# Performance work log

Hardware: AMD Instinct MI355X
Metric: run time of the kernel (lower is better)

The kernel has to match this reference:

```python
import jax, jax.numpy as jnp
import numpy as np

T, B, I, H = 4096, 32, 128, 128


def setup_inputs() -> dict:
    key = jax.random.key(0)
    ks = jax.random.split(key, 8)
    return {
        "input": jax.random.normal(ks[0], (T, B, I), dtype=jnp.float32),
        "h0": jax.random.normal(ks[1], (B, H), dtype=jnp.float32),
        "c0": jax.random.normal(ks[2], (B, H), dtype=jnp.float32),
        "noise": jax.random.normal(ks[3], (B, H), dtype=jnp.float32),
        "W_ih": jax.random.normal(ks[4], (4 * H, I), dtype=jnp.float32) * 0.05,
        "W_hh": jax.random.normal(ks[5], (4 * H, H), dtype=jnp.float32) * 0.05,
        "b_ih": jax.random.normal(ks[6], (4 * H,), dtype=jnp.float32) * 0.05,
        "b_hh": jax.random.normal(ks[7], (4 * H,), dtype=jnp.float32) * 0.05,
    }


def reference(input, h0, c0, noise, W_ih, W_hh, b_ih, b_hh):
    # NOTE: the source LSTMLayer never rebinds `state` inside its loop, so every
    # timestep applies the cell to the SAME initial (h0, c0). This is therefore a
    # time-batched (non-recurrent) LSTM-cell application -> fully vectorized over T.
    hsz = h0.shape[-1]
    # gates: [T, B, 4H]
    gates = (
        jnp.einsum("tbi,gi->tbg", input, W_ih)
        + jnp.einsum("bh,gh->bg", h0, W_hh)[None, :, :]
        + (b_ih + b_hh)
    )
    i_g = jax.nn.sigmoid(gates[..., 0 * hsz : 1 * hsz])
    f_g = jax.nn.sigmoid(gates[..., 1 * hsz : 2 * hsz])
    g_g = jnp.tanh(gates[..., 2 * hsz : 3 * hsz])
    o_g = jax.nn.sigmoid(gates[..., 3 * hsz : 4 * hsz])
    c = f_g * c0[None] + i_g * g_g               # [T, B, H]
    h = o_g * jnp.tanh(c) + noise[None]          # [T, B, H] (additive process noise)
    outputs = h
    # (h, c) returned by the torch loop are those of the LAST iteration
    return (outputs, (h[-1], c[-1]))
```

## Files before the change

kernel.cpp:

```cpp
#include <hip/hip_runtime.h>
#include <hip/hip_bf16.h>

#define T_DIM 4096
#define B_DIM 32
#define H_DIM 128
#define M_DIM (T_DIM * B_DIM)
#define G_DIM 512
#define TBH   ((long)M_DIM * H_DIM)

#define RPB    512
#define NCHUNK (RPB / 32)
#define LSTR   136
#define LBUF   (32 * LSTR)

typedef __attribute__((ext_vector_type(8))) short short8;
typedef __attribute__((ext_vector_type(4))) short short4v;
typedef __attribute__((ext_vector_type(4))) float floatx4;

__device__ __forceinline__ unsigned short f2bf_rne(float x) {
    union { float f; unsigned int u; } v; v.f = x;
    unsigned int r = v.u + 0x7FFFu + ((v.u >> 16) & 1u);
    return (unsigned short)(r >> 16);
}
__device__ __forceinline__ unsigned short f2bf_rh(float x) {
    union { float f; unsigned int u; } v; v.f = x;
    return (unsigned short)((v.u + 0x8000u) >> 16);
}
__device__ __forceinline__ float ex2(float x) { return __builtin_amdgcn_exp2f(x); }
__device__ __forceinline__ float rcpf(float x) { return __builtin_amdgcn_rcpf(x); }
__device__ __forceinline__ short8 pack8(float4 f0, float4 f1) {
    short8 s;
    s[0] = (short)f2bf_rh(f0.x); s[1] = (short)f2bf_rh(f0.y);
    s[2] = (short)f2bf_rh(f0.z); s[3] = (short)f2bf_rh(f0.w);
    s[4] = (short)f2bf_rh(f1.x); s[5] = (short)f2bf_rh(f1.y);
    s[6] = (short)f2bf_rh(f1.z); s[7] = (short)f2bf_rh(f1.w);
    return s;
}

__global__ void prep(const float* __restrict__ h0,
                     const float* __restrict__ W_hh,
                     const float* __restrict__ b_ih,
                     const float* __restrict__ b_hh,
                     const float* __restrict__ W_ih,
                     unsigned short* __restrict__ Wb,
                     float* __restrict__ hh) {
    const int tid = threadIdx.x;
    if (blockIdx.x < 32) {
        __shared__ float h0s[128];
        const int b = blockIdx.x;
        if (tid < 128) h0s[tid] = h0[b * 128 + tid];
        __syncthreads();
        for (int g = tid; g < G_DIM; g += 256) {
            float acc = b_ih[g] + b_hh[g];
            const float* wr = W_hh + g * 128;
            #pragma unroll 8
            for (int k = 0; k < 128; ++k) acc += wr[k] * h0s[k];
            hh[b * G_DIM + g] = acc;
        }
    } else {
        const int e = ((blockIdx.x - 32) * 256 + tid) * 4;
        float4 f = *(const float4*)(W_ih + e);
        short4v s;
        s[0] = (short)f2bf_rne(f.x); s[1] = (short)f2bf_rne(f.y);
        s[2] = (short)f2bf_rne(f.z); s[3] = (short)f2bf_rne(f.w);
        *(short4v*)(Wb + e) = s;
    }
}

__global__ __launch_bounds__(512, 2) void lstm_main(
    const float* __restrict__ X,
    const unsigned short* __restrict__ W,
    const float* __restrict__ hh,
    const float* __restrict__ c0,
    const float* __restrict__ noise,
    float* __restrict__ out)
{
    __shared__ unsigned short Xs[2 * LBUF];

    const int tid  = threadIdx.x;
    const int w    = tid >> 6;
    const int lane = tid & 63;
    const int q    = lane >> 4;
    const int lr   = lane & 15;
    const int hcol = (w << 4) + lr;
    const long row0 = (long)blockIdx.x * RPB;

    short8 wf[4][4];
    #pragma unroll
    for (int g = 0; g < 4; ++g)
        #pragma unroll
        for (int kt = 0; kt < 4; ++kt)
            wf[g][kt] = *(const short8*)(W + (g * 128 + hcol) * 128 + kt * 32 + q * 8);

    floatx4 hhf[2][4];
    float c0v[2][4], nzv[2][4];
    #pragma unroll
    for (int mt = 0; mt < 2; ++mt) {
        #pragma unroll
        for (int r = 0; r < 4; ++r) {
            const int b = mt * 16 + q * 4 + r;
            c0v[mt][r] = c0[b * 128 + hcol];
            nzv[mt][r] = noise[b * 128 + hcol];
        }
        #pragma unroll
        for (int g = 0; g < 4; ++g) {
            floatx4 a;
            #pragma unroll
            for (int r = 0; r < 4; ++r)
                a[r] = hh[(mt * 16 + q * 4 + r) * G_DIM + g * 128 + hcol];
            hhf[mt][g] = a;
        }
    }

    const int srow = tid >> 4;
    const int scol = (tid & 15) << 3;
    const float* xsrc = X + (row0 + srow) * 128 + scol;
    unsigned short* lws = &Xs[srow * LSTR + scol];

    {
        float4 f0 = *(const float4*)(xsrc);
        float4 f1 = *(const float4*)(xsrc + 4);
        *(short8*)lws = pack8(f0, f1);
    }
    float4 p0 = *(const float4*)(xsrc + 4096);
    float4 p1 = *(const float4*)(xsrc + 4096 + 4);
    __syncthreads();

    const float K1  = 1.44269504f;
    const float K2  = 2.88539008f;

    for (int c = 0; c < NCHUNK; ++c) {
        float4 n0 = {}, n1 = {};
        if (c + 2 < NCHUNK) {
            n0 = *(const float4*)(xsrc + (long)(c + 2) * 4096);
            n1 = *(const float4*)(xsrc + (long)(c + 2) * 4096 + 4);
        }

        const unsigned short* rb = &Xs[(c & 1) * LBUF];
        short8 af[2][4];
        #pragma unroll
        for (int mt = 0; mt < 2; ++mt)
            #pragma unroll
            for (int kt = 0; kt < 4; ++kt)
                af[mt][kt] = *(const short8*)(rb + (mt * 16 + lr) * LSTR + kt * 32 + q * 8);

        floatx4 acc[2][4];
        #pragma unroll
        for (int g = 0; g < 4; ++g) {
            acc[0][g] = __builtin_amdgcn_mfma_f32_16x16x32_bf16(af[0][0], wf[g][0], hhf[0][g], 0, 0, 0);
            acc[1][g] = __builtin_amdgcn_mfma_f32_16x16x32_bf16(af[1][0], wf[g][0], hhf[1][g], 0, 0, 0);
        }
        #pragma unroll
        for (int kt = 1; kt < 4; ++kt)
            #pragma unroll
            for (int g = 0; g < 4; ++g) {
                acc[0][g] = __builtin_amdgcn_mfma_f32_16x16x32_bf16(af[0][kt], wf[g][kt], acc[0][g], 0, 0, 0);
                acc[1][g] = __builtin_amdgcn_mfma_f32_16x16x32_bf16(af[1][kt], wf[g][kt], acc[1][g], 0, 0, 0);
            }

        const long rbase = row0 + (long)c * 32;
        const bool last = (rbase == M_DIM - 32);
        #pragma unroll
        for (int mt = 0; mt < 2; ++mt)
            #pragma unroll
            for (int r = 0; r < 4; ++r) {
                const long row = rbase + mt * 16 + q * 4 + r;
                const float ai = acc[mt][0][r];
                const float af_ = acc[mt][1][r];
                const float ag = acc[mt][2][r];
                const float ao = acc[mt][3][r];
                const float Ei = ex2(-K1 * ai);
                const float Ef = ex2(-K1 * af_);
                const float Eg = ex2( K2 * ag);
                const float Eo = ex2(-K1 * ao);
                const float ig = (Eg - 1.0f) * rcpf((1.0f + Ei) * (Eg + 1.0f));
                const float gf = rcpf(1.0f + Ef);
                const float cc = __builtin_fmaf(gf, c0v[mt][r], ig);
                const float Ec = ex2( K2 * cc);
                const float ot = (Ec - 1.0f) * rcpf((1.0f + Eo) * (Ec + 1.0f));
                const float hv = ot + nzv[mt][r];
                out[row * 128 + hcol] = hv;
                if (last) {
                    const int b = mt * 16 + q * 4 + r;
                    out[TBH +        b * 128 + hcol] = hv;
                    out[TBH + 4096 + b * 128 + hcol] = cc;
                }
            }

        if (c + 1 < NCHUNK)
            *(short8*)(lws + ((c + 1) & 1) * LBUF) = pack8(p0, p1);
        __syncthreads();
        p0 = n0; p1 = n1;
    }
}

extern "C" void kernel_launch(void* const* d_in, const int* in_sizes, int n_in,
                              void* d_out, int out_size, void* d_ws, size_t ws_size,
                              hipStream_t stream) {
    const float* X     = (const float*)d_in[0];
    const float* h0    = (const float*)d_in[1];
    const float* c0    = (const float*)d_in[2];
    const float* noise = (const float*)d_in[3];
    const float* W_ih  = (const float*)d_in[4];
    const float* W_hh  = (const float*)d_in[5];
    const float* b_ih  = (const float*)d_in[6];
    const float* b_hh  = (const float*)d_in[7];

    unsigned short* Wb = (unsigned short*)d_ws;
    float* hh = (float*)((char*)d_ws + 512 * 128 * sizeof(unsigned short));
    float* out = (float*)d_out;

    prep<<<dim3(96), dim3(256), 0, stream>>>(h0, W_hh, b_ih, b_hh, W_ih, Wb, hh);
    lstm_main<<<dim3(M_DIM / RPB), dim3(512), 0, stream>>>(X, Wb, hh, c0, noise, out);
}
```

Before: 149.7 us.

## Split LSTM gate computation across specialized wave groups with LDS handoff

Blocks grow to 1024 threads. Waves 0-7 compute the input and cell-candidate gates, convert the next X chunk to bf16 and write i*g to a double-buffered shared array. Waves 8-15 compute the forget and output gates, read i*g after the barrier, and do the cell/hidden activation and the global stores. This halves per-wave MFMA, register and transcendental work, and separates the load and store roles. The cost is extra LDS traffic, one more shared buffer, and a tighter coupling between the two wave groups at each barrier.

```diff
diff --git a/kernel.cpp b/kernel.cpp
--- a/kernel.cpp
+++ b/kernel.cpp
@@ -12,6 +12,9 @@
 #define NCHUNK (RPB / 32)
 #define LSTR   136
 #define LBUF   (32 * LSTR)
+#define IGSTR  20
+#define IGPAIR (32 * IGSTR)
+#define IGBUF  (8 * IGPAIR)
 
 typedef __attribute__((ext_vector_type(8))) short short8;
 typedef __attribute__((ext_vector_type(4))) short short4v;
@@ -67,7 +70,7 @@
     }
 }
 
-__global__ __launch_bounds__(512, 2) void lstm_main(
+__global__ __launch_bounds__(1024) void lstm_main(
     const float* __restrict__ X,
     const unsigned short* __restrict__ W,
     const float* __restrict__ hh,
@@ -76,40 +79,47 @@
     float* __restrict__ out)
 {
     __shared__ unsigned short Xs[2 * LBUF];
+    __shared__ float igs[2 * IGBUF];
 
     const int tid  = threadIdx.x;
     const int w    = tid >> 6;
     const int lane = tid & 63;
     const int q    = lane >> 4;
     const int lr   = lane & 15;
-    const int hcol = (w << 4) + lr;
+    const bool isA = (w < 8);
+    const int p    = w & 7;
+    const int bsel = w >> 3;
+    const int hcol = (p << 4) + lr;
     const long row0 = (long)blockIdx.x * RPB;
 
-    short8 wf[4][4];
+    short8 wf[2][4];
     #pragma unroll
-    for (int g = 0; g < 4; ++g)
+    for (int j = 0; j < 2; ++j)
         #pragma unroll
         for (int kt = 0; kt < 4; ++kt)
-            wf[g][kt] = *(const short8*)(W + (g * 128 + hcol) * 128 + kt * 32 + q * 8);
-
-    floatx4 hhf[2][4];
+            wf[j][kt] = *(const short8*)(W + (((j << 1) | bsel) * 128 + hcol) * 128 + kt * 32 + q * 8);
+
+    floatx4 hhf[2][2];
+    #pragma unroll
+    for (int mt = 0; mt < 2; ++mt)
+        #pragma unroll
+        for (int j = 0; j < 2; ++j) {
+            floatx4 a;
+            #pragma unroll
+            for (int r = 0; r < 4; ++r)
+                a[r] = hh[(mt * 16 + q * 4 + r) * G_DIM + ((j << 1) | bsel) * 128 + hcol];
+            hhf[mt][j] = a;
+        }
     float c0v[2][4], nzv[2][4];
-    #pragma unroll
-    for (int mt = 0; mt < 2; ++mt) {
-        #pragma unroll
-        for (int r = 0; r < 4; ++r) {
-            const int b = mt * 16 + q * 4 + r;
-            c0v[mt][r] = c0[b * 128 + hcol];
-            nzv[mt][r] = noise[b * 128 + hcol];
-        }
-        #pragma unroll
-        for (int g = 0; g < 4; ++g) {
-            floatx4 a;
-            #pragma unroll
-            for (int r = 0; r < 4; ++r)
-                a[r] = hh[(mt * 16 + q * 4 + r) * G_DIM + g * 128 + hcol];
-            hhf[mt][g] = a;
-        }
+    if (!isA) {
+        #pragma unroll
+        for (int mt = 0; mt < 2; ++mt)
+            #pragma unroll
+            for (int r = 0; r < 4; ++r) {
+                const int b = mt * 16 + q * 4 + r;
+                c0v[mt][r] = c0[b * 128 + hcol];
+                nzv[mt][r] = noise[b * 128 + hcol];
+            }
     }
 
     const int srow = tid >> 4;
@@ -117,25 +127,20 @@
     const float* xsrc = X + (row0 + srow) * 128 + scol;
     unsigned short* lws = &Xs[srow * LSTR + scol];
 
-    {
+    float4 p0 = {}, p1 = {}, n0 = {}, n1 = {};
+    if (isA) {
         float4 f0 = *(const float4*)(xsrc);
         float4 f1 = *(const float4*)(xsrc + 4);
         *(short8*)lws = pack8(f0, f1);
-    }
-    float4 p0 = *(const float4*)(xsrc + 4096);
-    float4 p1 = *(const float4*)(xsrc + 4096 + 4);
+        p0 = *(const float4*)(xsrc + 4096);
+        p1 = *(const float4*)(xsrc + 4096 + 4);
+    }
     __syncthreads();
 
-    const float K1  = 1.44269504f;
-    const float K2  = 2.88539008f;
+    const float K1 = 1.44269504f;
+    const float K2 = 2.88539008f;
 
     for (int c = 0; c < NCHUNK; ++c) {
-        float4 n0 = {}, n1 = {};
-        if (c + 2 < NCHUNK) {
-            n0 = *(const float4*)(xsrc + (long)(c + 2) * 4096);
-            n1 = *(const float4*)(xsrc + (long)(c + 2) * 4096 + 4);
-        }
-
         const unsigned short* rb = &Xs[(c & 1) * LBUF];
         short8 af[2][4];
         #pragma unroll
@@ -144,53 +149,71 @@
             for (int kt = 0; kt < 4; ++kt)
                 af[mt][kt] = *(const short8*)(rb + (mt * 16 + lr) * LSTR + kt * 32 + q * 8);
 
-        floatx4 acc[2][4];
-        #pragma unroll
-        for (int g = 0; g < 4; ++g) {
-            acc[0][g] = __builtin_amdgcn_mfma_f32_16x16x32_bf16(af[0][0], wf[g][0], hhf[0][g], 0, 0, 0);
-            acc[1][g] = __builtin_amdgcn_mfma_f32_16x16x32_bf16(af[1][0], wf[g][0], hhf[1][g], 0, 0, 0);
+        floatx4 acc[2][2];
+        #pragma unroll
+        for (int j = 0; j < 2; ++j) {
+            acc[0][j] = __builtin_amdgcn_mfma_f32_16x16x32_bf16(af[0][0], wf[j][0], hhf[0][j], 0, 0, 0);
+            acc[1][j] = __builtin_amdgcn_mfma_f32_16x16x32_bf16(af[1][0], wf[j][0], hhf[1][j], 0, 0, 0);
         }
         #pragma unroll
         for (int kt = 1; kt < 4; ++kt)
             #pragma unroll
-            for (int g = 0; g < 4; ++g) {
-                acc[0][g] = __builtin_amdgcn_mfma_f32_16x16x32_bf16(af[0][kt], wf[g][kt], acc[0][g], 0, 0, 0);
-                acc[1][g] = __builtin_amdgcn_mfma_f32_16x16x32_bf16(af[1][kt], wf[g][kt], acc[1][g], 0, 0, 0);
+            for (int j = 0; j < 2; ++j) {
+                acc[0][j] = __builtin_amdgcn_mfma_f32_16x16x32_bf16(af[0][kt], wf[j][kt], acc[0][j], 0, 0, 0);
+                acc[1][j] = __builtin_amdgcn_mfma_f32_16x16x32_bf16(af[1][kt], wf[j][kt], acc[1][j], 0, 0, 0);
             }
 
-        const long rbase = row0 + (long)c * 32;
-        const bool last = (rbase == M_DIM - 32);
-        #pragma unroll
-        for (int mt = 0; mt < 2; ++mt)
-            #pragma unroll
-            for (int r = 0; r < 4; ++r) {
-                const long row = rbase + mt * 16 + q * 4 + r;
-                const float ai = acc[mt][0][r];
-                const float af_ = acc[mt][1][r];
-                const float ag = acc[mt][2][r];
-                const float ao = acc[mt][3][r];
-                const float Ei = ex2(-K1 * ai);
-                const float Ef = ex2(-K1 * af_);
-                const float Eg = ex2( K2 * ag);
-                const float Eo = ex2(-K1 * ao);
-                const float ig = (Eg - 1.0f) * rcpf((1.0f + Ei) * (Eg + 1.0f));
-                const float gf = rcpf(1.0f + Ef);
-                const float cc = __builtin_fmaf(gf, c0v[mt][r], ig);
-                const float Ec = ex2( K2 * cc);
-                const float ot = (Ec - 1.0f) * rcpf((1.0f + Eo) * (Ec + 1.0f));
-                const float hv = ot + nzv[mt][r];
-                out[row * 128 + hcol] = hv;
-                if (last) {
-                    const int b = mt * 16 + q * 4 + r;
-                    out[TBH +        b * 128 + hcol] = hv;
-                    out[TBH + 4096 + b * 128 + hcol] = cc;
+        if (isA) {
+            if (c + 2 < NCHUNK) {
+                n0 = *(const float4*)(xsrc + (long)(c + 2) * 4096);
+                n1 = *(const float4*)(xsrc + (long)(c + 2) * 4096 + 4);
+            }
+            float* igw = &igs[(c & 1) * IGBUF + p * IGPAIR + (q * 4) * IGSTR + lr];
+            #pragma unroll
+            for (int mt = 0; mt < 2; ++mt)
+                #pragma unroll
+                for (int r = 0; r < 4; ++r) {
+                    const float ai = acc[mt][0][r];
+                    const float ag = acc[mt][1][r];
+                    const float Ei = ex2(-K1 * ai);
+                    const float Eg = ex2( K2 * ag);
+                    igw[(mt * 16 + r) * IGSTR] =
+                        (Eg - 1.0f) * rcpf((1.0f + Ei) * (Eg + 1.0f));
                 }
-            }
-
-        if (c + 1 < NCHUNK)
-            *(short8*)(lws + ((c + 1) & 1) * LBUF) = pack8(p0, p1);
+            if (c + 1 < NCHUNK)
+                *(short8*)(lws + ((c + 1) & 1) * LBUF) = pack8(p0, p1);
+        }
         __syncthreads();
-        p0 = n0; p1 = n1;
+
+        if (!isA) {
+            const float* igr = &igs[(c & 1) * IGBUF + p * IGPAIR + (q * 4) * IGSTR + lr];
+            const long rbase = row0 + (long)c * 32;
+            const bool last = (rbase == M_DIM - 32);
+            #pragma unroll
+            for (int mt = 0; mt < 2; ++mt)
+                #pragma unroll
+                for (int r = 0; r < 4; ++r) {
+                    const long row = rbase + mt * 16 + q * 4 + r;
+                    const float ig = igr[(mt * 16 + r) * IGSTR];
+                    const float afv = acc[mt][0][r];
+                    const float ao  = acc[mt][1][r];
+                    const float Ef = ex2(-K1 * afv);
+                    const float gf = rcpf(1.0f + Ef);
+                    const float cc = __builtin_fmaf(gf, c0v[mt][r], ig);
+                    const float Ec = ex2( K2 * cc);
+                    const float Eo = ex2(-K1 * ao);
+                    const float ot = (Ec - 1.0f) * rcpf((1.0f + Eo) * (Ec + 1.0f));
+                    const float hv = ot + nzv[mt][r];
+                    out[row * 128 + hcol] = hv;
+                    if (last) {
+                        const int b = mt * 16 + q * 4 + r;
+                        out[TBH +        b * 128 + hcol] = hv;
+                        out[TBH + 4096 + b * 128 + hcol] = cc;
+                    }
+                }
+        } else {
+            p0 = n0; p1 = n1;
+        }
     }
 }
 
@@ -211,5 +234,5 @@
     float* out = (float*)d_out;
 
     prep<<<dim3(96), dim3(256), 0, stream>>>(h0, W_hh, b_ih, b_hh, W_ih, Wb, hh);
-    lstm_main<<<dim3(M_DIM / RPB), dim3(512), 0, stream>>>(X, Wb, hh, c0, noise, out);
-}
+    lstm_main<<<dim3(M_DIM / RPB), dim3(1024), 0, stream>>>(X, Wb, hh, c0, noise, out);
+}
```

After: 155.7 us. 4.1% more time.
